# Kernel optimization log

Hardware: AMD Instinct MI355X
Metric: run time of the kernel (lower is better)

Reference implementation:

```python
import jax, jax.numpy as jnp
import numpy as np

B, T, H, D = 1, 4096, 8, 64
CHUNK = 1024
SCALE = 0.125  # 1/sqrt(head_size)
EPS = 1e-6


def setup_inputs() -> dict:
    key = jax.random.key(0)
    k1, k2, k3, k4 = jax.random.split(key, 4)
    q = jax.random.normal(k1, (B, T, H, D), jnp.float32)
    k = jax.random.normal(k2, (B, T, H, D), jnp.float32)
    v = jax.random.normal(k3, (B, T, H, D), jnp.float32)
    # log gates: small negative values (log of per-token decay in (0,1])
    log_g = -0.05 * jax.random.uniform(k4, (B, T, H), jnp.float32)
    return {"q": q, "k": k, "v": v, "log_g": log_g}


def _power_retention(q, k, v, log_g):
    """Chunked degree-2 power retention with log-gating.

    score(t,s) = exp(g_t - g_s) * (scale * q_t . k_s)^2  (causal),
    where g = cumsum(log_g). Cross-chunk part carried via expanded state
    S[h,d,e,v] = sum_s w_s k_d k_e v  (phi(k) = k (x) k, since (q.k)^2 = phi(q).phi(k))
    and sum-of-keys normalizer s[h,d,e]. out = num / max(den, eps).
    """
    Bq, Tq, Hq, Dq = q.shape
    C, L = Tq // CHUNK, CHUNK
    qs = (q * SCALE).reshape(Bq, C, L, Hq, Dq)   # fold scale into q
    kc = k.reshape(Bq, C, L, Hq, Dq)
    vc = v.reshape(Bq, C, L, Hq, Dq)
    g = jnp.cumsum(log_g.reshape(Bq, C, L, Hq), axis=2)  # [B,C,L,H] in-chunk cum gate
    g_end = g[:, :, -1, :]                                # [B,C,H]

    # ---- intra-chunk (parallel form) ----
    scores = jnp.einsum('bclhd,bcshd->bclsh', qs, kc)          # [B,C,L,S,H]
    logdec = g[:, :, :, None, :] - g[:, :, None, :, :]          # g_t - g_s
    causal = jnp.arange(L)[:, None] >= jnp.arange(L)[None, :]
    A = jnp.where(causal[None, None, :, :, None],
                  jnp.exp(logdec) * scores * scores, 0.0)       # [B,C,L,S,H]
    intra = jnp.einsum('bclsh,bcshv->bclhv', A, vc)             # [B,C,L,H,Dv]
    row = A.sum(axis=3)                                         # [B,C,L,H]

    # ---- per-chunk state contributions ----
    wk = jnp.exp(g_end[:, :, None, :] - g)                      # key-side decay to chunk end
    kw = kc * wk[..., None]
    P = jnp.einsum('bclhd,bclhe,bclhv->bchdev', kw, kc, vc)     # [B,C,H,D,D,Dv]
    Z = jnp.einsum('bclhd,bclhe->bchde', kw, kc)                # [B,C,H,D,D]
    qdec = jnp.exp(g)                                           # query-side decay from chunk start
    gtot = jnp.exp(g_end)                                       # whole-chunk decay

    def step(carry, xs):
        S, sk = carry
        qc, Pc, Zc, gd, gt = xs   # qc [B,L,H,D], Pc [B,H,D,D,Dv], gd [B,L,H], gt [B,H]
        inter = jnp.einsum('blhd,blhe,bhdev->blhv', qc, qc, S) * gd[..., None]
        den_i = jnp.einsum('blhd,blhe,bhde->blh', qc, qc, sk) * gd
        S = gt[:, :, None, None, None] * S + Pc
        sk = gt[:, :, None, None] * sk + Zc
        return (S, sk), (inter, den_i)

    S0 = jnp.zeros((Bq, Hq, Dq, Dq, Dq), q.dtype)
    sk0 = jnp.zeros((Bq, Hq, Dq, Dq), q.dtype)
    xs = (jnp.moveaxis(qs, 1, 0), jnp.moveaxis(P, 1, 0), jnp.moveaxis(Z, 1, 0),
          jnp.moveaxis(qdec, 1, 0), jnp.moveaxis(gtot, 1, 0))
    (_, _), (inter, den_i) = jax.lax.scan(step, (S0, sk0), xs)
    inter = jnp.moveaxis(inter, 0, 1)   # [B,C,L,H,Dv]
    den_i = jnp.moveaxis(den_i, 0, 1)   # [B,C,L,H]

    num = intra + inter
    den = jnp.maximum(row + den_i, EPS)
    out = num / den[..., None]
    return out.reshape(Bq, Tq, Hq, Dq)


def reference(q, k, v, log_g):
    return _power_retention(q, k, v, log_g)
```

## Files before the change

kernel.cpp:

```cpp
#include <hip/hip_runtime.h>
#include <math.h>

typedef float f32x4 __attribute__((ext_vector_type(4)));
typedef __bf16 bf16x8 __attribute__((ext_vector_type(8)));
typedef __bf16 bf16x4 __attribute__((ext_vector_type(4)));

namespace {
constexpr int NC = 4, CL = 1024, NH = 8, ND = 64;
constexpr float KSCALE = 0.125f, KEPS = 1e-6f;
constexpr int PQ = 72;
constexpr int PK = 40;
}

#define MFMA(a,b,c) __builtin_amdgcn_mfma_f32_16x16x32_bf16((a),(b),(c),0,0,0)

__global__ __launch_bounds__(1024) void gate_kernel(const float* __restrict__ lg,
    float* __restrict__ g_arr, float* __restrict__ gend, float* __restrict__ gtot) {
  int c = blockIdx.x >> 3, h = blockIdx.x & 7;
  int l = threadIdx.x;
  __shared__ float sm[CL];
  sm[l] = lg[(c*CL + l)*NH + h];
  __syncthreads();
  for (int off = 1; off < CL; off <<= 1) {
    float t = (l >= off) ? sm[l-off] : 0.f;
    __syncthreads();
    sm[l] += t;
    __syncthreads();
  }
  g_arr[(c*NH + h)*CL + l] = sm[l];
  if (l == 0) { gend[c*NH+h] = sm[CL-1]; gtot[c*NH+h] = expf(sm[CL-1]); }
}

__global__ __launch_bounds__(256) void convert_kernel(const float* __restrict__ q,
    const float* __restrict__ k, const float* __restrict__ v,
    const float* __restrict__ g_arr, const float* __restrict__ gend,
    __bf16* __restrict__ qgb, __bf16* __restrict__ kgb,
    __bf16* __restrict__ kht, __bf16* __restrict__ vt) {
  int lt = blockIdx.x, h = blockIdx.y, c = blockIdx.z;
  int ch = c*NH + h;
  int t = threadIdx.x;
  __shared__ float ld[64][65];
  int lr = t >> 2, sg = t & 3;
  int l = lt*64 + lr;
  size_t ib = ((size_t)(c*CL + l)*NH + h)*ND + sg*16;
  float ge = gend[ch];
  float gl = g_arr[ch*CL + l];
  float eq = expf(0.5f*gl), ekk = expf(-0.5f*gl), ew = expf(0.5f*(ge-gl));
  float qv[16], kv[16], vv[16];
  #pragma unroll
  for (int i = 0; i < 4; ++i) {
    *(f32x4*)&qv[4*i] = *(const f32x4*)&q[ib+4*i];
    *(f32x4*)&kv[4*i] = *(const f32x4*)&k[ib+4*i];
    *(f32x4*)&vv[4*i] = *(const f32x4*)&v[ib+4*i];
  }
  size_t ob = ((size_t)ch*CL + l)*ND + sg*16;
  {
    bf16x8 a, b;
    #pragma unroll
    for (int i = 0; i < 8; ++i) { a[i]=(__bf16)(qv[i]*KSCALE*eq); b[i]=(__bf16)(qv[8+i]*KSCALE*eq); }
    *(bf16x8*)&qgb[ob] = a; *(bf16x8*)&qgb[ob+8] = b;
    #pragma unroll
    for (int i = 0; i < 8; ++i) { a[i]=(__bf16)(kv[i]*ekk); b[i]=(__bf16)(kv[8+i]*ekk); }
    *(bf16x8*)&kgb[ob] = a; *(bf16x8*)&kgb[ob+8] = b;
  }
  #pragma unroll
  for (int i = 0; i < 16; ++i) ld[lr][sg*16+i] = kv[i]*ew;
  __syncthreads();
  {
    int d = t >> 2, s2 = t & 3;
    bf16x8 a, b;
    #pragma unroll
    for (int i = 0; i < 8; ++i) { a[i]=(__bf16)ld[s2*16+i][d]; b[i]=(__bf16)ld[s2*16+8+i][d]; }
    size_t kb = ((size_t)ch*ND + d)*CL + lt*64 + s2*16;
    *(bf16x8*)&kht[kb] = a; *(bf16x8*)&kht[kb+8] = b;
  }
  __syncthreads();
  #pragma unroll
  for (int i = 0; i < 16; ++i) ld[lr][sg*16+i] = vv[i];
  __syncthreads();
  {
    int p = t >> 2, s2 = t & 3;
    bf16x8 a, b;
    #pragma unroll
    for (int i = 0; i < 8; ++i) { a[i]=(__bf16)ld[s2*16+i][p]; b[i]=(__bf16)ld[s2*16+8+i][p]; }
    size_t vb = ((size_t)ch*80 + p)*CL + lt*64 + s2*16;
    *(bf16x8*)&vt[vb] = a; *(bf16x8*)&vt[vb+8] = b;
  }
  if (t < 64) vt[((size_t)ch*80 + 64)*CL + lt*64 + t] = (__bf16)1.0f;
  for (int idx = t; idx < 15*64; idx += 256)
    vt[((size_t)ch*80 + 65 + idx/64)*CL + lt*64 + (idx & 63)] = (__bf16)0.0f;
}

__global__ __launch_bounds__(256) void intra_kernel(const __bf16* __restrict__ qgb,
    const __bf16* __restrict__ kgb, const __bf16* __restrict__ vt,
    float* __restrict__ out, float* __restrict__ rowp) {
  int rt = blockIdx.x, h = blockIdx.y, c = blockIdx.z;
  int ch = c*NH + h;
  int t = threadIdx.x, wv = t >> 6, lane = t & 63, qq = lane >> 4, lm = lane & 15;
  __shared__ __align__(16) __bf16 qt[64*PQ];
  __shared__ __align__(16) __bf16 kgl[2][32*PQ];
  __shared__ __align__(16) __bf16 vtl[2][80*PK];
  __shared__ __align__(16) __bf16 As[64*PK];
  int nst = 2*rt + 2;
  int r8 = t >> 3, sg8 = t & 7;
  int r4 = t >> 2, s4 = t & 3;
  bf16x8 rkg, rva, rvb;
  auto load_it = [&](int s3) {
    rkg = *(const bf16x8*)&kgb[((size_t)ch*CL + s3*32 + r8)*ND + sg8*8];
    rva = *(const bf16x8*)&vt[((size_t)ch*80 + r4)*CL + s3*32 + s4*8];
    if (t < 64) rvb = *(const bf16x8*)&vt[((size_t)ch*80 + 64 + r4)*CL + s3*32 + s4*8];
  };
  auto write_it = [&](int buf) {
    *(bf16x8*)&kgl[buf][r8*PQ + sg8*8] = rkg;
    *(bf16x8*)&vtl[buf][r4*PK + s4*8] = rva;
    if (t < 64) *(bf16x8*)&vtl[buf][(64+r4)*PK + s4*8] = rvb;
  };
  {
    int r = t >> 2, sg = t & 3;
    size_t gb = ((size_t)ch*CL + rt*64 + r)*ND + sg*16;
    *(bf16x8*)&qt[r*PQ + sg*16]     = *(const bf16x8*)&qgb[gb];
    *(bf16x8*)&qt[r*PQ + sg*16 + 8] = *(const bf16x8*)&qgb[gb+8];
  }
  load_it(0);
  write_it(0);
  __syncthreads();
  bf16x8 bq0 = *(bf16x8*)&qt[(wv*16+lm)*PQ + qq*8];
  bf16x8 bq1 = *(bf16x8*)&qt[(wv*16+lm)*PQ + 32 + qq*8];
  f32x4 acc[5];
  #pragma unroll
  for (int n = 0; n < 5; ++n) acc[n] = (f32x4){0.f,0.f,0.f,0.f};
  int r_gc = rt*64 + wv*16 + lm;
  int buf = 0;
  for (int s3 = 0; s3 < nst; ++s3) {
    if (s3 + 1 < nst) load_it(s3 + 1);
    #pragma unroll
    for (int ss = 0; ss < 2; ++ss) {
      f32x4 dr = (f32x4){0.f,0.f,0.f,0.f};
      bf16x8 a0 = *(bf16x8*)&kgl[buf][(ss*16+lm)*PQ + qq*8];
      bf16x8 a1 = *(bf16x8*)&kgl[buf][(ss*16+lm)*PQ + 32 + qq*8];
      dr = MFMA(a0, bq0, dr);
      dr = MFMA(a1, bq1, dr);
      bf16x4 pk;
      #pragma unroll
      for (int j = 0; j < 4; ++j) {
        int s_g = s3*32 + ss*16 + qq*4 + j;
        float dv = dr[j];
        pk[j] = (__bf16)((s_g <= r_gc) ? dv*dv : 0.f);
      }
      *(bf16x4*)&As[(wv*16+lm)*PK + ss*16 + qq*4] = pk;
    }
    bf16x8 aav = *(bf16x8*)&As[(wv*16+lm)*PK + qq*8];
    #pragma unroll
    for (int n = 0; n < 5; ++n) {
      bf16x8 bv = *(bf16x8*)&vtl[buf][(n*16+lm)*PK + qq*8];
      acc[n] = MFMA(aav, bv, acc[n]);
    }
    if (s3 + 1 < nst) write_it(buf ^ 1);
    __syncthreads();
    buf ^= 1;
  }
  if (c == 0) {
    #pragma unroll
    for (int j = 0; j < 4; ++j) {
      float rs = __shfl(acc[4][j], lane & 48, 64);
      float dinv = 1.f / fmaxf(rs, KEPS);
      int rg = rt*64 + wv*16 + qq*4 + j;
      size_t ob = ((size_t)(c*CL + rg)*NH + h)*ND + lm;
      #pragma unroll
      for (int n = 0; n < 4; ++n) out[ob + 16*n] = acc[n][j]*dinv;
    }
  } else {
    #pragma unroll
    for (int j = 0; j < 4; ++j) {
      int rg = rt*64 + wv*16 + qq*4 + j;
      size_t ob = ((size_t)(c*CL + rg)*NH + h)*ND + lm;
      #pragma unroll
      for (int n = 0; n < 4; ++n) out[ob + 16*n] = acc[n][j];
      if (lm == 0) rowp[ch*CL + rg] = acc[4][j];
    }
  }
}

__global__ __launch_bounds__(256) void pzscan_kernel(const __bf16* __restrict__ kht,
    const __bf16* __restrict__ vt, const float* __restrict__ gtot,
    __bf16* __restrict__ st) {
  int mblk = blockIdx.x, h = blockIdx.y;
  int t = threadIdx.x, wv = t >> 6, lane = t & 63, qq = lane >> 4, lm = lane & 15;
  __shared__ __align__(16) __bf16 ke[2][64*PK];
  __shared__ __align__(16) __bf16 kd[2][2*PK];
  __shared__ __align__(16) __bf16 vtl[2][80*PK];
  __shared__ float tb[64][72];
  int dl = wv >> 1, e0w = (wv & 1)*32;
  int r = t >> 2, cg = t & 3;
  bf16x8 rke, rva, rvb, rkd;
  auto load_it = [&](int it) {
    int cc = it >> 5, kk = it & 31;
    int ch = cc*NH + h;
    int l0 = kk*32;
    rke = *(const bf16x8*)&kht[((size_t)ch*ND + r)*CL + l0 + cg*8];
    rva = *(const bf16x8*)&vt[((size_t)ch*80 + r)*CL + l0 + cg*8];
    if (t < 64) rvb = *(const bf16x8*)&vt[((size_t)ch*80 + 64 + r)*CL + l0 + cg*8];
    if (t < 8)  rkd = *(const bf16x8*)&kht[((size_t)ch*ND + mblk*2 + (t>>2))*CL + l0 + (t&3)*8];
  };
  auto write_it = [&](int buf) {
    *(bf16x8*)&ke[buf][r*PK + cg*8] = rke;
    *(bf16x8*)&vtl[buf][r*PK + cg*8] = rva;
    if (t < 64) *(bf16x8*)&vtl[buf][(64+r)*PK + cg*8] = rvb;
    if (t < 8)  *(bf16x8*)&kd[buf][(t>>2)*PK + (t&3)*8] = rkd;
  };
  f32x4 S_reg[2][5], acc[2][5];
  #pragma unroll
  for (int m = 0; m < 2; ++m)
    #pragma unroll
    for (int n = 0; n < 5; ++n) {
      S_reg[m][n] = (f32x4){0.f,0.f,0.f,0.f};
      acc[m][n] = (f32x4){0.f,0.f,0.f,0.f};
    }
  load_it(0);
  write_it(0);
  __syncthreads();
  int buf = 0;
  for (int it = 0; it < 96; ++it) {
    if (it < 95) load_it(it + 1);
    bf16x8 kd8 = *(bf16x8*)&kd[buf][dl*PK + qq*8];
    bf16x8 am[2];
    #pragma unroll
    for (int m = 0; m < 2; ++m) {
      bf16x8 ke8 = *(bf16x8*)&ke[buf][(e0w + 16*m + lm)*PK + qq*8];
      bf16x8 a;
      #pragma unroll
      for (int i = 0; i < 8; ++i) a[i] = (__bf16)((float)kd8[i] * (float)ke8[i]);
      am[m] = a;
    }
    #pragma unroll
    for (int n = 0; n < 5; ++n) {
      bf16x8 bv = *(bf16x8*)&vtl[buf][(16*n+lm)*PK + qq*8];
      acc[0][n] = MFMA(am[0], bv, acc[0][n]);
      acc[1][n] = MFMA(am[1], bv, acc[1][n]);
    }
    if (it < 95) write_it(buf ^ 1);
    __syncthreads();
    buf ^= 1;
    if ((it & 31) == 31) {
      int cc = it >> 5;
      float gt = gtot[cc*NH + h];
      #pragma unroll
      for (int m = 0; m < 2; ++m)
        #pragma unroll
        for (int n = 0; n < 5; ++n)
          #pragma unroll
          for (int j = 0; j < 4; ++j) {
            S_reg[m][n][j] = gt*S_reg[m][n][j] + acc[m][n][j];
            acc[m][n][j] = 0.f;
          }
      size_t slab = (size_t)(cc*NH + h)*80;
      for (int h2 = 0; h2 < 2; ++h2) {
        __syncthreads();
        if (dl == h2) {
          #pragma unroll
          for (int m = 0; m < 2; ++m)
            #pragma unroll
            for (int n = 0; n < 4; ++n)
              #pragma unroll
              for (int j = 0; j < 4; ++j)
                tb[e0w + 16*m + qq*4 + j][16*n + lm] = S_reg[m][n][j];
        }
        __syncthreads();
        {
          int vr = t >> 2, es = t & 3;
          bf16x8 a, b;
          #pragma unroll
          for (int i = 0; i < 8; ++i) { a[i]=(__bf16)tb[es*16+i][vr]; b[i]=(__bf16)tb[es*16+8+i][vr]; }
          size_t sb = (slab + vr)*4096 + (size_t)(mblk*2 + h2)*64 + es*16;
          *(bf16x8*)&st[sb] = a; *(bf16x8*)&st[sb+8] = b;
        }
      }
      if (lm == 0) {
        #pragma unroll
        for (int m = 0; m < 2; ++m)
          #pragma unroll
          for (int j = 0; j < 4; ++j)
            st[(slab + 64)*4096 + (size_t)(mblk*2 + dl)*64 + e0w + 16*m + qq*4 + j] =
              (__bf16)S_reg[m][4][j];
      }
    }
  }
}

__global__ __launch_bounds__(256) void inter_partial_kernel(
    const __bf16* __restrict__ qgb, const __bf16* __restrict__ st,
    float* __restrict__ pnum, float* __restrict__ pden) {
  int mb = blockIdx.x;
  int ks = blockIdx.y;
  int hc = blockIdx.z;
  int slab = hc >> 3, h = hc & 7;
  int c = slab + 1, ch = c*NH + h;
  int t = threadIdx.x, wv = t >> 6, lane = t & 63, qq = lane >> 4, lm = lane & 15;
  __shared__ __align__(16) __bf16 stl[2][65*PQ];
  size_t slabbase = (size_t)(slab*NH + h)*80;
  int rrow = mb*64 + wv*16 + lm;
  size_t qb = ((size_t)ch*CL + rrow)*ND;
  bf16x8 qe0 = *(const bf16x8*)&qgb[qb + qq*8];
  bf16x8 qe1 = *(const bf16x8*)&qgb[qb + 32 + qq*8];
  float qd[16];
  {
    bf16x8 qa = *(const bf16x8*)&qgb[qb + ks*16];
    bf16x8 qbv = *(const bf16x8*)&qgb[qb + ks*16 + 8];
    #pragma unroll
    for (int i = 0; i < 8; ++i) { qd[i] = (float)qa[i]; qd[8+i] = (float)qbv[i]; }
  }
  int r = t >> 2, cg = t & 3;
  bf16x8 sa, sb, sc;
  auto load_ph = [&](int ph) {
    size_t base = (slabbase + r)*4096 + (size_t)(ks*16 + ph)*64 + cg*16;
    sa = *(const bf16x8*)&st[base];
    sb = *(const bf16x8*)&st[base + 8];
    if (t < 8) sc = *(const bf16x8*)&st[(slabbase + 64)*4096 + (size_t)(ks*16 + ph)*64 + t*8];
  };
  auto write_ph = [&](int buf) {
    *(bf16x8*)&stl[buf][r*PQ + cg*16]     = sa;
    *(bf16x8*)&stl[buf][r*PQ + cg*16 + 8] = sb;
    if (t < 8) *(bf16x8*)&stl[buf][64*PQ + t*8] = sc;
  };
  f32x4 acc[5];
  #pragma unroll
  for (int n = 0; n < 5; ++n) acc[n] = (f32x4){0.f,0.f,0.f,0.f};
  load_ph(0);
  write_ph(0);
  __syncthreads();
  #pragma unroll
  for (int ph = 0; ph < 16; ++ph) {
    int buf = ph & 1;
    if (ph < 15) load_ph(ph + 1);
    float qdv = qd[ph];
    #pragma unroll
    for (int s = 0; s < 2; ++s) {
      bf16x8 qe = s ? qe1 : qe0;
      bf16x8 a;
      #pragma unroll
      for (int i = 0; i < 8; ++i) a[i] = (__bf16)(qdv * (float)qe[i]);
      #pragma unroll
      for (int n = 0; n < 5; ++n) {
        bf16x8 bv = *(bf16x8*)&stl[buf][(16*n + lm)*PQ + s*32 + qq*8];
        acc[n] = MFMA(a, bv, acc[n]);
      }
    }
    if (ph < 15) write_ph(buf ^ 1);
    __syncthreads();
  }
  size_t prow = (size_t)hc*1024 + mb*64 + wv*16;
  #pragma unroll
  for (int j = 0; j < 4; ++j) {
    int rloc = qq*4 + j;
    #pragma unroll
    for (int n = 0; n < 4; ++n)
      atomicAdd(&pnum[(prow + rloc)*64 + 16*n + lm], acc[n][j]);
    if (lm == 0) atomicAdd(&pden[prow + rloc], acc[4][j]);
  }
}

__global__ __launch_bounds__(256) void finalize_kernel(const float* __restrict__ rowp,
    const float* __restrict__ pnum, const float* __restrict__ pden,
    float* __restrict__ out) {
  int idx = blockIdx.x*256 + threadIdx.x;
  int e4 = idx*4;
  int row = e4 >> 6;
  int col = e4 & 63;
  int hc = row >> 10, rg = row & 1023;
  int slab = hc >> 3, h = hc & 7, c = slab + 1;
  float dinv = 1.f / fmaxf(rowp[(c*NH + h)*CL + rg] + pden[row], KEPS);
  f32x4 pv = *(const f32x4*)&pnum[e4];
  size_t ob = ((size_t)(c*CL + rg)*NH + h)*ND + col;
  f32x4 ov = *(const f32x4*)&out[ob];
  #pragma unroll
  for (int j = 0; j < 4; ++j) ov[j] = (ov[j] + pv[j]) * dinv;
  *(f32x4*)&out[ob] = ov;
}

extern "C" void kernel_launch(void* const* d_in, const int* in_sizes, int n_in,
                              void* d_out, int out_size, void* d_ws, size_t ws_size,
                              hipStream_t stream) {
  const float* q  = (const float*)d_in[0];
  const float* k  = (const float*)d_in[1];
  const float* v  = (const float*)d_in[2];
  const float* lg = (const float*)d_in[3];
  float* out = (float*)d_out;

  float* wf    = (float*)d_ws;
  float* g_arr = wf;
  float* gend  = g_arr + 32768;
  float* gtot  = gend + 32;
  float* rowp  = gtot + 32;
  float* pden  = rowp + 32768;
  float* pnum  = pden + 24576;
  __bf16* qgb  = (__bf16*)(pnum + 1572864);
  __bf16* kgb  = qgb + 2097152;
  __bf16* kht  = kgb + 2097152;
  __bf16* vt   = kht + 2097152;
  __bf16* st   = vt + 2621440;

  hipMemsetAsync(pden, 0, (size_t)(24576 + 1572864)*sizeof(float), stream);
  gate_kernel<<<dim3(NC*NH), dim3(CL), 0, stream>>>(lg, g_arr, gend, gtot);
  convert_kernel<<<dim3(16, NH, NC), dim3(256), 0, stream>>>(q, k, v, g_arr, gend, qgb, kgb, kht, vt);
  intra_kernel<<<dim3(16, NH, NC), dim3(256), 0, stream>>>(qgb, kgb, vt, out, rowp);
  pzscan_kernel<<<dim3(32, NH), dim3(256), 0, stream>>>(kht, vt, gtot, st);
  inter_partial_kernel<<<dim3(16, 4, 24), dim3(256), 0, stream>>>(qgb, st, pnum, pden);
  finalize_kernel<<<dim3(1536), dim3(256), 0, stream>>>(rowp, pnum, pden, out);
}
```

Before: 215.6 us.

## Balance intra-chunk work and split state scan into parallel per-chunk build plus scan

```diff
diff --git a/kernel.cpp b/kernel.cpp
--- a/kernel.cpp
+++ b/kernel.cpp
@@ -93,15 +93,15 @@
 
 __global__ __launch_bounds__(256) void intra_kernel(const __bf16* __restrict__ qgb,
     const __bf16* __restrict__ kgb, const __bf16* __restrict__ vt,
-    float* __restrict__ out, float* __restrict__ rowp) {
-  int rt = blockIdx.x, h = blockIdx.y, c = blockIdx.z;
+    float* __restrict__ pnum, float* __restrict__ pden) {
+  int p = blockIdx.x, hf = blockIdx.y;
+  int h = blockIdx.z & 7, c = blockIdx.z >> 3;
   int ch = c*NH + h;
   int t = threadIdx.x, wv = t >> 6, lane = t & 63, qq = lane >> 4, lm = lane & 15;
   __shared__ __align__(16) __bf16 qt[64*PQ];
   __shared__ __align__(16) __bf16 kgl[2][32*PQ];
   __shared__ __align__(16) __bf16 vtl[2][80*PK];
   __shared__ __align__(16) __bf16 As[64*PK];
-  int nst = 2*rt + 2;
   int r8 = t >> 3, sg8 = t & 7;
   int r4 = t >> 2, s4 = t & 3;
   bf16x8 rkg, rva, rvb;
@@ -115,176 +115,159 @@
     *(bf16x8*)&vtl[buf][r4*PK + s4*8] = rva;
     if (t < 64) *(bf16x8*)&vtl[buf][(64+r4)*PK + s4*8] = rvb;
   };
-  {
-    int r = t >> 2, sg = t & 3;
-    size_t gb = ((size_t)ch*CL + rt*64 + r)*ND + sg*16;
-    *(bf16x8*)&qt[r*PQ + sg*16]     = *(const bf16x8*)&qgb[gb];
-    *(bf16x8*)&qt[r*PQ + sg*16 + 8] = *(const bf16x8*)&qgb[gb+8];
-  }
-  load_it(0);
-  write_it(0);
-  __syncthreads();
-  bf16x8 bq0 = *(bf16x8*)&qt[(wv*16+lm)*PQ + qq*8];
-  bf16x8 bq1 = *(bf16x8*)&qt[(wv*16+lm)*PQ + 32 + qq*8];
-  f32x4 acc[5];
-  #pragma unroll
-  for (int n = 0; n < 5; ++n) acc[n] = (f32x4){0.f,0.f,0.f,0.f};
-  int r_gc = rt*64 + wv*16 + lm;
-  int buf = 0;
-  for (int s3 = 0; s3 < nst; ++s3) {
-    if (s3 + 1 < nst) load_it(s3 + 1);
-    #pragma unroll
-    for (int ss = 0; ss < 2; ++ss) {
-      f32x4 dr = (f32x4){0.f,0.f,0.f,0.f};
-      bf16x8 a0 = *(bf16x8*)&kgl[buf][(ss*16+lm)*PQ + qq*8];
-      bf16x8 a1 = *(bf16x8*)&kgl[buf][(ss*16+lm)*PQ + 32 + qq*8];
-      dr = MFMA(a0, bq0, dr);
-      dr = MFMA(a1, bq1, dr);
-      bf16x4 pk;
-      #pragma unroll
-      for (int j = 0; j < 4; ++j) {
-        int s_g = s3*32 + ss*16 + qq*4 + j;
-        float dv = dr[j];
-        pk[j] = (__bf16)((s_g <= r_gc) ? dv*dv : 0.f);
+  for (int ph = 0; ph < 2; ++ph) {
+    int rt = ph ? (15 - p) : p;
+    int ntile = rt + 1;
+    int s_beg = hf * ntile;
+    {
+      int r = t >> 2, sg = t & 3;
+      size_t gb = ((size_t)ch*CL + rt*64 + r)*ND + sg*16;
+      *(bf16x8*)&qt[r*PQ + sg*16]     = *(const bf16x8*)&qgb[gb];
+      *(bf16x8*)&qt[r*PQ + sg*16 + 8] = *(const bf16x8*)&qgb[gb+8];
+    }
+    load_it(s_beg);
+    write_it(0);
+    __syncthreads();
+    bf16x8 bq0 = *(bf16x8*)&qt[(wv*16+lm)*PQ + qq*8];
+    bf16x8 bq1 = *(bf16x8*)&qt[(wv*16+lm)*PQ + 32 + qq*8];
+    f32x4 acc[5];
+    #pragma unroll
+    for (int n = 0; n < 5; ++n) acc[n] = (f32x4){0.f,0.f,0.f,0.f};
+    int r_gc = rt*64 + wv*16 + lm;
+    int buf = 0;
+    for (int ii = 0; ii < ntile; ++ii) {
+      int s3 = s_beg + ii;
+      if (ii + 1 < ntile) load_it(s3 + 1);
+      #pragma unroll
+      for (int ss = 0; ss < 2; ++ss) {
+        f32x4 dr = (f32x4){0.f,0.f,0.f,0.f};
+        bf16x8 a0 = *(bf16x8*)&kgl[buf][(ss*16+lm)*PQ + qq*8];
+        bf16x8 a1 = *(bf16x8*)&kgl[buf][(ss*16+lm)*PQ + 32 + qq*8];
+        dr = MFMA(a0, bq0, dr);
+        dr = MFMA(a1, bq1, dr);
+        bf16x4 pk;
+        #pragma unroll
+        for (int j = 0; j < 4; ++j) {
+          int s_g = s3*32 + ss*16 + qq*4 + j;
+          float dv = dr[j];
+          pk[j] = (__bf16)((s_g <= r_gc) ? dv*dv : 0.f);
+        }
+        *(bf16x4*)&As[(wv*16+lm)*PK + ss*16 + qq*4] = pk;
       }
-      *(bf16x4*)&As[(wv*16+lm)*PK + ss*16 + qq*4] = pk;
-    }
-    bf16x8 aav = *(bf16x8*)&As[(wv*16+lm)*PK + qq*8];
-    #pragma unroll
-    for (int n = 0; n < 5; ++n) {
-      bf16x8 bv = *(bf16x8*)&vtl[buf][(n*16+lm)*PK + qq*8];
-      acc[n] = MFMA(aav, bv, acc[n]);
-    }
-    if (s3 + 1 < nst) write_it(buf ^ 1);
-    __syncthreads();
-    buf ^= 1;
-  }
-  if (c == 0) {
-    #pragma unroll
-    for (int j = 0; j < 4; ++j) {
-      float rs = __shfl(acc[4][j], lane & 48, 64);
-      float dinv = 1.f / fmaxf(rs, KEPS);
-      int rg = rt*64 + wv*16 + qq*4 + j;
-      size_t ob = ((size_t)(c*CL + rg)*NH + h)*ND + lm;
-      #pragma unroll
-      for (int n = 0; n < 4; ++n) out[ob + 16*n] = acc[n][j]*dinv;
-    }
-  } else {
+      bf16x8 aav = *(bf16x8*)&As[(wv*16+lm)*PK + qq*8];
+      #pragma unroll
+      for (int n = 0; n < 5; ++n) {
+        bf16x8 bv = *(bf16x8*)&vtl[buf][(n*16+lm)*PK + qq*8];
+        acc[n] = MFMA(aav, bv, acc[n]);
+      }
+      if (ii + 1 < ntile) write_it(buf ^ 1);
+      __syncthreads();
+      buf ^= 1;
+    }
     #pragma unroll
     for (int j = 0; j < 4; ++j) {
       int rg = rt*64 + wv*16 + qq*4 + j;
-      size_t ob = ((size_t)(c*CL + rg)*NH + h)*ND + lm;
-      #pragma unroll
-      for (int n = 0; n < 4; ++n) out[ob + 16*n] = acc[n][j];
-      if (lm == 0) rowp[ch*CL + rg] = acc[4][j];
-    }
-  }
-}
-
-__global__ __launch_bounds__(256) void pzscan_kernel(const __bf16* __restrict__ kht,
-    const __bf16* __restrict__ vt, const float* __restrict__ gtot,
-    __bf16* __restrict__ st) {
-  int mblk = blockIdx.x, h = blockIdx.y;
+      size_t base = ((size_t)ch*CL + rg)*64 + lm;
+      #pragma unroll
+      for (int n = 0; n < 4; ++n) atomicAdd(&pnum[base + 16*n], acc[n][j]);
+      if (lm == 0) atomicAdd(&pden[ch*CL + rg], acc[4][j]);
+    }
+    __syncthreads();
+  }
+}
+
+__global__ __launch_bounds__(256) void pz_kernel(const __bf16* __restrict__ kht,
+    const __bf16* __restrict__ vt, __bf16* __restrict__ st) {
+  int dd = blockIdx.x, h = blockIdx.y, cc = blockIdx.z;
+  int ch = cc*NH + h;
   int t = threadIdx.x, wv = t >> 6, lane = t & 63, qq = lane >> 4, lm = lane & 15;
-  __shared__ __align__(16) __bf16 ke[2][64*PK];
-  __shared__ __align__(16) __bf16 kd[2][2*PK];
-  __shared__ __align__(16) __bf16 vtl[2][80*PK];
-  __shared__ float tb[64][72];
-  int dl = wv >> 1, e0w = (wv & 1)*32;
+  constexpr int KE_SZ = 2*64*PK;
+  constexpr int KD_SZ = 2*PK;
+  constexpr int VT_SZ = 2*80*PK;
+  __shared__ __align__(16) __bf16 smem[KE_SZ + KD_SZ + VT_SZ];
+  __bf16 (*ke)[64*PK]  = reinterpret_cast<__bf16(*)[64*PK]>(&smem[0]);
+  __bf16 (*kd)[PK]     = reinterpret_cast<__bf16(*)[PK]>(&smem[KE_SZ]);
+  __bf16 (*vtl)[80*PK] = reinterpret_cast<__bf16(*)[80*PK]>(&smem[KE_SZ + KD_SZ]);
+  float  (*tb)[65]     = reinterpret_cast<float(*)[65]>(&smem[0]);
   int r = t >> 2, cg = t & 3;
   bf16x8 rke, rva, rvb, rkd;
-  auto load_it = [&](int it) {
-    int cc = it >> 5, kk = it & 31;
-    int ch = cc*NH + h;
+  auto load_it = [&](int kk) {
     int l0 = kk*32;
     rke = *(const bf16x8*)&kht[((size_t)ch*ND + r)*CL + l0 + cg*8];
     rva = *(const bf16x8*)&vt[((size_t)ch*80 + r)*CL + l0 + cg*8];
     if (t < 64) rvb = *(const bf16x8*)&vt[((size_t)ch*80 + 64 + r)*CL + l0 + cg*8];
-    if (t < 8)  rkd = *(const bf16x8*)&kht[((size_t)ch*ND + mblk*2 + (t>>2))*CL + l0 + (t&3)*8];
+    if (t < 4)  rkd = *(const bf16x8*)&kht[((size_t)ch*ND + dd)*CL + l0 + t*8];
   };
   auto write_it = [&](int buf) {
     *(bf16x8*)&ke[buf][r*PK + cg*8] = rke;
     *(bf16x8*)&vtl[buf][r*PK + cg*8] = rva;
     if (t < 64) *(bf16x8*)&vtl[buf][(64+r)*PK + cg*8] = rvb;
-    if (t < 8)  *(bf16x8*)&kd[buf][(t>>2)*PK + (t&3)*8] = rkd;
-  };
-  f32x4 S_reg[2][5], acc[2][5];
-  #pragma unroll
-  for (int m = 0; m < 2; ++m)
-    #pragma unroll
-    for (int n = 0; n < 5; ++n) {
-      S_reg[m][n] = (f32x4){0.f,0.f,0.f,0.f};
-      acc[m][n] = (f32x4){0.f,0.f,0.f,0.f};
-    }
+    if (t < 4)  *(bf16x8*)&kd[buf][t*8] = rkd;
+  };
+  f32x4 acc[5];
+  #pragma unroll
+  for (int n = 0; n < 5; ++n) acc[n] = (f32x4){0.f,0.f,0.f,0.f};
   load_it(0);
   write_it(0);
   __syncthreads();
   int buf = 0;
-  for (int it = 0; it < 96; ++it) {
-    if (it < 95) load_it(it + 1);
-    bf16x8 kd8 = *(bf16x8*)&kd[buf][dl*PK + qq*8];
-    bf16x8 am[2];
-    #pragma unroll
-    for (int m = 0; m < 2; ++m) {
-      bf16x8 ke8 = *(bf16x8*)&ke[buf][(e0w + 16*m + lm)*PK + qq*8];
-      bf16x8 a;
-      #pragma unroll
-      for (int i = 0; i < 8; ++i) a[i] = (__bf16)((float)kd8[i] * (float)ke8[i]);
-      am[m] = a;
-    }
+  for (int kk = 0; kk < 32; ++kk) {
+    if (kk < 31) load_it(kk + 1);
+    bf16x8 kd8 = *(bf16x8*)&kd[buf][qq*8];
+    bf16x8 ke8 = *(bf16x8*)&ke[buf][(wv*16+lm)*PK + qq*8];
+    bf16x8 a;
+    #pragma unroll
+    for (int i = 0; i < 8; ++i) a[i] = (__bf16)((float)kd8[i] * (float)ke8[i]);
     #pragma unroll
     for (int n = 0; n < 5; ++n) {
       bf16x8 bv = *(bf16x8*)&vtl[buf][(16*n+lm)*PK + qq*8];
-      acc[0][n] = MFMA(am[0], bv, acc[0][n]);
-      acc[1][n] = MFMA(am[1], bv, acc[1][n]);
-    }
-    if (it < 95) write_it(buf ^ 1);
+      acc[n] = MFMA(a, bv, acc[n]);
+    }
+    if (kk < 31) write_it(buf ^ 1);
     __syncthreads();
     buf ^= 1;
-    if ((it & 31) == 31) {
-      int cc = it >> 5;
-      float gt = gtot[cc*NH + h];
-      #pragma unroll
-      for (int m = 0; m < 2; ++m)
-        #pragma unroll
-        for (int n = 0; n < 5; ++n)
-          #pragma unroll
-          for (int j = 0; j < 4; ++j) {
-            S_reg[m][n][j] = gt*S_reg[m][n][j] + acc[m][n][j];
-            acc[m][n][j] = 0.f;
-          }
-      size_t slab = (size_t)(cc*NH + h)*80;
-      for (int h2 = 0; h2 < 2; ++h2) {
-        __syncthreads();
-        if (dl == h2) {
-          #pragma unroll
-          for (int m = 0; m < 2; ++m)
-            #pragma unroll
-            for (int n = 0; n < 4; ++n)
-              #pragma unroll
-              for (int j = 0; j < 4; ++j)
-                tb[e0w + 16*m + qq*4 + j][16*n + lm] = S_reg[m][n][j];
-        }
-        __syncthreads();
-        {
-          int vr = t >> 2, es = t & 3;
-          bf16x8 a, b;
-          #pragma unroll
-          for (int i = 0; i < 8; ++i) { a[i]=(__bf16)tb[es*16+i][vr]; b[i]=(__bf16)tb[es*16+8+i][vr]; }
-          size_t sb = (slab + vr)*4096 + (size_t)(mblk*2 + h2)*64 + es*16;
-          *(bf16x8*)&st[sb] = a; *(bf16x8*)&st[sb+8] = b;
-        }
-      }
-      if (lm == 0) {
-        #pragma unroll
-        for (int m = 0; m < 2; ++m)
-          #pragma unroll
-          for (int j = 0; j < 4; ++j)
-            st[(slab + 64)*4096 + (size_t)(mblk*2 + dl)*64 + e0w + 16*m + qq*4 + j] =
-              (__bf16)S_reg[m][4][j];
-      }
-    }
-  }
+  }
+  #pragma unroll
+  for (int n = 0; n < 4; ++n)
+    #pragma unroll
+    for (int j = 0; j < 4; ++j)
+      tb[wv*16 + qq*4 + j][16*n + lm] = acc[n][j];
+  __syncthreads();
+  {
+    int vr = t >> 2, es = t & 3;
+    bf16x8 a, b;
+    #pragma unroll
+    for (int i = 0; i < 8; ++i) { a[i] = (__bf16)tb[es*16+i][vr]; b[i] = (__bf16)tb[es*16+8+i][vr]; }
+    size_t sb = ((size_t)ch*80 + vr)*4096 + (size_t)dd*64 + es*16;
+    *(bf16x8*)&st[sb] = a; *(bf16x8*)&st[sb+8] = b;
+  }
+  if (lm == 0) {
+    #pragma unroll
+    for (int j = 0; j < 4; ++j)
+      st[((size_t)ch*80 + 64)*4096 + (size_t)dd*64 + wv*16 + qq*4 + j] = (__bf16)acc[4][j];
+  }
+}
+
+__global__ __launch_bounds__(256) void scan_kernel(const float* __restrict__ gtot,
+    __bf16* __restrict__ st) {
+  int h = blockIdx.y;
+  size_t off = ((size_t)blockIdx.x*256 + threadIdx.x)*8;
+  float g1 = gtot[NH + h], g2 = gtot[2*NH + h];
+  size_t b0 = ((size_t)(0*NH + h)*80)*4096 + off;
+  size_t b1 = ((size_t)(1*NH + h)*80)*4096 + off;
+  size_t b2 = ((size_t)(2*NH + h)*80)*4096 + off;
+  bf16x8 p0 = *(bf16x8*)&st[b0];
+  bf16x8 p1 = *(bf16x8*)&st[b1];
+  bf16x8 p2 = *(bf16x8*)&st[b2];
+  bf16x8 o1, o2;
+  #pragma unroll
+  for (int i = 0; i < 8; ++i) {
+    float v1 = g1*(float)p0[i] + (float)p1[i];
+    o1[i] = (__bf16)v1;
+    o2[i] = (__bf16)(g2*v1 + (float)p2[i]);
+  }
+  *(bf16x8*)&st[b1] = o1;
+  *(bf16x8*)&st[b2] = o2;
 }
 
 __global__ __launch_bounds__(256) void inter_partial_kernel(
@@ -348,7 +331,7 @@
     if (ph < 15) write_ph(buf ^ 1);
     __syncthreads();
   }
-  size_t prow = (size_t)hc*1024 + mb*64 + wv*16;
+  size_t prow = (size_t)ch*CL + mb*64 + wv*16;
   #pragma unroll
   for (int j = 0; j < 4; ++j) {
     int rloc = qq*4 + j;
@@ -359,21 +342,20 @@
   }
 }
 
-__global__ __launch_bounds__(256) void finalize_kernel(const float* __restrict__ rowp,
-    const float* __restrict__ pnum, const float* __restrict__ pden,
-    float* __restrict__ out) {
+__global__ __launch_bounds__(256) void finalize_kernel(const float* __restrict__ pnum,
+    const float* __restrict__ pden, float* __restrict__ out) {
   int idx = blockIdx.x*256 + threadIdx.x;
   int e4 = idx*4;
   int row = e4 >> 6;
   int col = e4 & 63;
   int hc = row >> 10, rg = row & 1023;
-  int slab = hc >> 3, h = hc & 7, c = slab + 1;
-  float dinv = 1.f / fmaxf(rowp[(c*NH + h)*CL + rg] + pden[row], KEPS);
+  int c = hc >> 3, h = hc & 7;
+  float dinv = 1.f / fmaxf(pden[row], KEPS);
   f32x4 pv = *(const f32x4*)&pnum[e4];
   size_t ob = ((size_t)(c*CL + rg)*NH + h)*ND + col;
-  f32x4 ov = *(const f32x4*)&out[ob];
-  #pragma unroll
-  for (int j = 0; j < 4; ++j) ov[j] = (ov[j] + pv[j]) * dinv;
+  f32x4 ov;
+  #pragma unroll
+  for (int j = 0; j < 4; ++j) ov[j] = pv[j] * dinv;
   *(f32x4*)&out[ob] = ov;
 }
 
@@ -390,20 +372,20 @@
   float* g_arr = wf;
   float* gend  = g_arr + 32768;
   float* gtot  = gend + 32;
-  float* rowp  = gtot + 32;
-  float* pden  = rowp + 32768;
-  float* pnum  = pden + 24576;
-  __bf16* qgb  = (__bf16*)(pnum + 1572864);
+  float* pden  = gtot + 32;
+  float* pnum  = pden + 32768;
+  __bf16* qgb  = (__bf16*)(pnum + 2097152);
   __bf16* kgb  = qgb + 2097152;
   __bf16* kht  = kgb + 2097152;
   __bf16* vt   = kht + 2097152;
   __bf16* st   = vt + 2621440;
 
-  hipMemsetAsync(pden, 0, (size_t)(24576 + 1572864)*sizeof(float), stream);
+  hipMemsetAsync(pden, 0, (size_t)(32768 + 2097152)*sizeof(float), stream);
   gate_kernel<<<dim3(NC*NH), dim3(CL), 0, stream>>>(lg, g_arr, gend, gtot);
   convert_kernel<<<dim3(16, NH, NC), dim3(256), 0, stream>>>(q, k, v, g_arr, gend, qgb, kgb, kht, vt);
-  intra_kernel<<<dim3(16, NH, NC), dim3(256), 0, stream>>>(qgb, kgb, vt, out, rowp);
-  pzscan_kernel<<<dim3(32, NH), dim3(256), 0, stream>>>(kht, vt, gtot, st);
+  intra_kernel<<<dim3(8, 2, 32), dim3(256), 0, stream>>>(qgb, kgb, vt, pnum, pden);
+  pz_kernel<<<dim3(64, NH, 3), dim3(256), 0, stream>>>(kht, vt, st);
+  scan_kernel<<<dim3(160, NH), dim3(256), 0, stream>>>(gtot, st);
   inter_partial_kernel<<<dim3(16, 4, 24), dim3(256), 0, stream>>>(qgb, st, pnum, pden);
-  finalize_kernel<<<dim3(1536), dim3(256), 0, stream>>>(rowp, pnum, pden, out);
-}
+  finalize_kernel<<<dim3(2048), dim3(256), 0, stream>>>(pnum, pden, out);
+}
```

Result: faster. 196.1 us (-9.0%).
